# Kernel optimization log

Hardware: AMD Instinct MI355X
Metric: run time of the kernel (lower is better)

The kernel has to match this reference:

```python
import jax, jax.numpy as jnp
import numpy as np

D_MODEL = 512
NUM_HEADS = 8
D_FF = 2048
HEAD_DIM = D_MODEL // NUM_HEADS
EPS = 1e-8


def rmsnorm(x, scale):
    rms = jax.lax.rsqrt(jnp.mean(x * x, axis=-1, keepdims=True) + EPS)
    return scale * x * rms


def alibi_bias(seq_len, num_heads):
    # faithful to: 1.0 / (arange(1,H+1) * 2**arange(0,8)[:,None]).flatten()[:H]
    a = jnp.arange(1, num_heads + 1, dtype=jnp.float32)          # (H,)
    b = 2.0 ** jnp.arange(0, 8, dtype=jnp.float32)[:, None]       # (8,1)
    slopes = (1.0 / (a * b).reshape(-1))[:num_heads]               # (H,)
    pos = jnp.arange(seq_len)
    dist = jnp.abs(pos[:, None] - pos[None, :]).astype(jnp.float32)  # (S,S)
    return -slopes[:, None, None] * dist[None]                     # (H,S,S)


def setup_inputs() -> dict:
    key = jax.random.key(0)
    ks = jax.random.split(key, 12)
    s = 0.02
    return {
        "x": jax.random.normal(ks[0], (2, 2048, D_MODEL), dtype=jnp.float32),
        "norm1_scale": jnp.ones((D_MODEL,), jnp.float32),
        "norm2_scale": jnp.ones((D_MODEL,), jnp.float32),
        "in_proj_w": jax.random.normal(ks[1], (3 * D_MODEL, D_MODEL), jnp.float32) * s,
        "in_proj_b": jnp.zeros((3 * D_MODEL,), jnp.float32),
        "out_proj_w": jax.random.normal(ks[2], (D_MODEL, D_MODEL), jnp.float32) * s,
        "out_proj_b": jnp.zeros((D_MODEL,), jnp.float32),
        "w1": jax.random.normal(ks[3], (D_FF, D_MODEL), jnp.float32) * s,
        "b1": jnp.zeros((D_FF,), jnp.float32),
        "w2": jax.random.normal(ks[4], (D_MODEL, D_FF), jnp.float32) * s,
        "b2": jnp.zeros((D_MODEL,), jnp.float32),
    }


def reference(x, norm1_scale, norm2_scale, in_proj_w, in_proj_b,
              out_proj_w, out_proj_b, w1, b1, w2, b2):
    B, S, D = x.shape
    xn = rmsnorm(x, norm1_scale)
    qkv = xn @ in_proj_w.T + in_proj_b                      # (B,S,3D)
    q, k, v = jnp.split(qkv, 3, axis=-1)
    q = q.reshape(B, S, NUM_HEADS, HEAD_DIM)
    k = k.reshape(B, S, NUM_HEADS, HEAD_DIM)
    v = v.reshape(B, S, NUM_HEADS, HEAD_DIM)
    scale = 1.0 / jnp.sqrt(jnp.float32(HEAD_DIM))
    scores = jnp.einsum('bqhd,bkhd->bhqk', q, k) * scale    # (B,H,S,S)
    scores = scores + alibi_bias(S, NUM_HEADS)[None]
    attn = jax.nn.softmax(scores, axis=-1)
    ctx = jnp.einsum('bhqk,bkhd->bqhd', attn, v).reshape(B, S, D)
    attn_out = ctx @ out_proj_w.T + out_proj_b
    x = x + attn_out                                        # dropout is identity (eval)
    xn2 = rmsnorm(x, norm2_scale)
    h = jax.nn.gelu(xn2 @ w1.T + b1, approximate=False)
    mlp_out = h @ w2.T + b2
    return x + mlp_out
```

## Files before the change

kernel.cpp:

```cpp
#include <hip/hip_runtime.h>
#include <math.h>


typedef __bf16 bf16x8 __attribute__((ext_vector_type(8)));
typedef float  f32x4  __attribute__((ext_vector_type(4)));

#define TOKENS 4096
#define DMODEL 512
#define SEQ    2048
#define SPLITK 2
#define QSCALE 0.1803368801f

__device__ __forceinline__ void gl_lds16(const __bf16* g, __bf16* l) {
    __builtin_amdgcn_global_load_lds(
        (const __attribute__((address_space(1))) void*)g,
        (__attribute__((address_space(3))) void*)l, 16, 0, 0);
}

union PkU { unsigned u; __bf16 h[2]; };

__global__ void pre_kernel(const float* __restrict__ x, const float* __restrict__ n1s,
                           __bf16* __restrict__ xn1,
                           const float* __restrict__ w0, const float* __restrict__ w1,
                           const float* __restrict__ w2, const float* __restrict__ w3,
                           __bf16* __restrict__ d0, __bf16* __restrict__ d1,
                           __bf16* __restrict__ d2, __bf16* __restrict__ d3) {
    if (blockIdx.x < 1024) {
        int wave = threadIdx.x >> 6, lane = threadIdx.x & 63;
        int tok = blockIdx.x * 4 + wave;
        const float* row = x + (size_t)tok * DMODEL;
        float4 v0 = *(const float4*)&row[lane * 4];
        float4 v1 = *(const float4*)&row[256 + lane * 4];
        float ss = v0.x*v0.x + v0.y*v0.y + v0.z*v0.z + v0.w*v0.w
                 + v1.x*v1.x + v1.y*v1.y + v1.z*v1.z + v1.w*v1.w;
        #pragma unroll
        for (int off = 1; off < 64; off <<= 1) ss += __shfl_xor(ss, off);
        float r = rsqrtf(ss * (1.0f / DMODEL) + 1e-8f);
        __bf16* o = xn1 + (size_t)tok * DMODEL;
        o[lane*4 + 0] = (__bf16)(v0.x * r * n1s[lane*4 + 0]);
        o[lane*4 + 1] = (__bf16)(v0.y * r * n1s[lane*4 + 1]);
        o[lane*4 + 2] = (__bf16)(v0.z * r * n1s[lane*4 + 2]);
        o[lane*4 + 3] = (__bf16)(v0.w * r * n1s[lane*4 + 3]);
        o[256 + lane*4 + 0] = (__bf16)(v1.x * r * n1s[256 + lane*4 + 0]);
        o[256 + lane*4 + 1] = (__bf16)(v1.y * r * n1s[256 + lane*4 + 1]);
        o[256 + lane*4 + 2] = (__bf16)(v1.z * r * n1s[256 + lane*4 + 2]);
        o[256 + lane*4 + 3] = (__bf16)(v1.w * r * n1s[256 + lane*4 + 3]);
    } else {
        const int N0 = 1536 * 512, N1 = 512 * 512, N2 = 2048 * 512, N3 = 512 * 2048;
        int i4 = ((blockIdx.x - 1024) * 256 + threadIdx.x) * 4;
        const float* s; __bf16* d;
        if (i4 < N0)              { s = w0 + i4;  d = d0 + i4; }
        else if ((i4 -= N0) < N1) { s = w1 + i4;  d = d1 + i4; }
        else if ((i4 -= N1) < N2) { s = w2 + i4;  d = d2 + i4; }
        else if ((i4 -= N2) < N3) { s = w3 + i4;  d = d3 + i4; }
        else return;
        float4 v = *(const float4*)s;
        d[0] = (__bf16)v.x; d[1] = (__bf16)v.y; d[2] = (__bf16)v.z; d[3] = (__bf16)v.w;
    }
}

__global__ void rmsnorm_kernel(const float* __restrict__ x, const float* __restrict__ scale,
                               __bf16* __restrict__ out) {
    int wave = threadIdx.x >> 6, lane = threadIdx.x & 63;
    int tok = blockIdx.x * 4 + wave;
    const float* row = x + (size_t)tok * DMODEL;
    float4 v0 = *(const float4*)&row[lane * 4];
    float4 v1 = *(const float4*)&row[256 + lane * 4];
    float ss = v0.x*v0.x + v0.y*v0.y + v0.z*v0.z + v0.w*v0.w
             + v1.x*v1.x + v1.y*v1.y + v1.z*v1.z + v1.w*v1.w;
    #pragma unroll
    for (int off = 1; off < 64; off <<= 1) ss += __shfl_xor(ss, off);
    float r = rsqrtf(ss * (1.0f / DMODEL) + 1e-8f);
    __bf16* o = out + (size_t)tok * DMODEL;
    o[lane*4 + 0] = (__bf16)(v0.x * r * scale[lane*4 + 0]);
    o[lane*4 + 1] = (__bf16)(v0.y * r * scale[lane*4 + 1]);
    o[lane*4 + 2] = (__bf16)(v0.z * r * scale[lane*4 + 2]);
    o[lane*4 + 3] = (__bf16)(v0.w * r * scale[lane*4 + 3]);
    o[256 + lane*4 + 0] = (__bf16)(v1.x * r * scale[256 + lane*4 + 0]);
    o[256 + lane*4 + 1] = (__bf16)(v1.y * r * scale[256 + lane*4 + 1]);
    o[256 + lane*4 + 2] = (__bf16)(v1.z * r * scale[256 + lane*4 + 2]);
    o[256 + lane*4 + 3] = (__bf16)(v1.w * r * scale[256 + lane*4 + 3]);
}

template <int EPI, int TM>
__global__ __launch_bounds__(256) void gemm_bt(
    const __bf16* __restrict__ A, const __bf16* __restrict__ W,
    const float* __restrict__ bias, const float* __restrict__ res,
    float* __restrict__ Cf, __bf16* __restrict__ Cb,
    __bf16* __restrict__ qb, __bf16* __restrict__ kb, __bf16* __restrict__ vtb,
    int M, int N, int K)
{
    constexpr int RI = TM / 32;
    __shared__ alignas(16) __bf16 As[2][TM * 32];
    __shared__ alignas(16) __bf16 Bs[2][128 * 32];
    const int tid = threadIdx.x;
    const int bm = blockIdx.x * TM;
    const int bn = blockIdx.y * 128;
    const int wave = tid >> 6, lane = tid & 63;
    const int wm = (wave & 1) * (TM / 2), wn = (wave >> 1) * 64;
    const int lrow = lane & 15;
    const int kq = (lane >> 4) * 8;

    f32x4 acc[RI][4] = {};

    for (int k0 = 0; k0 < K; k0 += 64) {
        __syncthreads();
        #pragma unroll
        for (int i = 0; i < TM / 32; i++) {
            int tt = i * 256 + tid;
            int kh = tt / (TM * 4), rem = tt % (TM * 4);
            int mrow = rem >> 2, c8 = rem & 3;
            gl_lds16(&A[(size_t)(bm + mrow) * K + k0 + kh * 32 + c8 * 8],
                     (__bf16*)As + tt * 8);
        }
        #pragma unroll
        for (int i = 0; i < 4; i++) {
            int tt = i * 256 + tid;
            int kh = tt >> 9, rem = tt & 511;
            int nrow = rem >> 2, c8 = rem & 3;
            gl_lds16(&W[(size_t)(bn + nrow) * K + k0 + kh * 32 + c8 * 8],
                     (__bf16*)Bs + tt * 8);
        }
        __syncthreads();
        #pragma unroll
        for (int kh = 0; kh < 2; kh++) {
            bf16x8 af[RI], bfv[4];
            #pragma unroll
            for (int i = 0; i < RI; i++) af[i] = *(bf16x8*)&As[kh][(wm + i*16 + lrow)*32 + kq];
            #pragma unroll
            for (int j = 0; j < 4; j++) bfv[j] = *(bf16x8*)&Bs[kh][(wn + j*16 + lrow)*32 + kq];
            #pragma unroll
            for (int i = 0; i < RI; i++)
                #pragma unroll
                for (int j = 0; j < 4; j++)
                    acc[i][j] = __builtin_amdgcn_mfma_f32_16x16x32_bf16(af[i], bfv[j], acc[i][j], 0, 0, 0);
        }
    }

    const int crow0 = (lane >> 4) * 4;
    const int ccol = lane & 15;
    const int quad = lane >> 4;

    if (EPI == 4) {
        #pragma unroll
        for (int j = 0; j < 4; j++) {
            const int col = bn + wn + j * 16 + ccol;
            const float bv = bias[col];
            if (col < 512) {
                const int h = col >> 6, d = col & 63;
                #pragma unroll
                for (int i = 0; i < RI; i++) {
                    const int row0 = bm + wm + i * 16 + crow0;
                    const int b = row0 >> 11, s0 = row0 & 2047;
                    #pragma unroll
                    for (int r = 0; r < 4; r++)
                        qb[(((size_t)b*8 + h)*2048 + s0 + r)*64 + d] =
                            (__bf16)((acc[i][j][r] + bv) * QSCALE);
                }
            } else if (col < 1024) {
                const int h = (col - 512) >> 6, d = col & 63;
                #pragma unroll
                for (int i = 0; i < RI; i++) {
                    const int row0 = bm + wm + i * 16 + crow0;
                    const int b = row0 >> 11, s0 = row0 & 2047;
                    #pragma unroll
                    for (int r = 0; r < 4; r++)
                        kb[(((size_t)b*8 + h)*2048 + s0 + r)*64 + d] = (__bf16)(acc[i][j][r] + bv);
                }
            } else {
                const int h = (col - 1024) >> 6, d = col & 63;
                const int tok0 = bm + wm;
                const int b = tok0 >> 11, sbase = tok0 & 2047;
                unsigned* vrow = (unsigned*)vtb + (((size_t)b*8 + h)*64 + d) * 1024 + (sbase >> 1);
                #pragma unroll
                for (int ip = 0; ip < RI / 2; ip++) {
                    #pragma unroll
                    for (int r = 0; r < 4; r++) {
                        PkU pk;
                        pk.h[0] = (__bf16)(acc[2*ip][j][r] + bv);
                        pk.h[1] = (__bf16)(acc[2*ip+1][j][r] + bv);
                        vrow[ip * 16 + quad * 4 + r] = pk.u;
                    }
                }
            }
        }
    } else {
        #pragma unroll
        for (int i = 0; i < RI; i++) {
            const int row0 = bm + wm + i * 16 + crow0;
            #pragma unroll
            for (int j = 0; j < 4; j++) {
                const int col = bn + wn + j * 16 + ccol;
                const float bv = bias[col];
                if (EPI == 1) {
                    #pragma unroll
                    for (int r = 0; r < 4; r++) {
                        const size_t idx = (size_t)(row0 + r) * N + col;
                        Cf[idx] = res[idx] + acc[i][j][r] + bv;
                    }
                } else {
                    #pragma unroll
                    for (int r = 0; r < 4; r++) {
                        float v = acc[i][j][r] + bv;
                        Cb[(size_t)(row0 + r) * N + col] =
                            (__bf16)(0.5f * v * (1.0f + erff(v * 0.70710678f)));
                    }
                }
            }
        }
    }
}

__global__ __launch_bounds__(256, 4) void attn_kernel(
    const __bf16* __restrict__ qb, const __bf16* __restrict__ kb,
    const __bf16* __restrict__ vtb,
    __bf16* __restrict__ Opart, float* __restrict__ lpart)
{
    const int qt = blockIdx.x, bh = blockIdx.y, sp = blockIdx.z;
    const int h = bh & 7;
    const int tid = threadIdx.x, wave = tid >> 6, lane = tid & 63;
    const int lrow = lane & 15, quad = lane >> 4;

    __shared__ alignas(16) __bf16 Ks[2][2][64 * 32];
    __shared__ alignas(16) __bf16 Vt[2][2][64 * 32];
    __shared__ alignas(16) unsigned Pt4[4][2][32][20];

    const float slope2 = -1.44269504f / (float)(h + 1);
    const int qbase = qt * 128 + wave * 32;
    const int kt0 = sp * (32 / SPLITK), kt1 = kt0 + 32 / SPLITK;

    bf16x8 qf[2][2];
    #pragma unroll
    for (int rt = 0; rt < 2; rt++)
        #pragma unroll
        for (int dh = 0; dh < 2; dh++)
            qf[rt][dh] = *(const bf16x8*)&qb[((size_t)bh*2048 + qbase + rt*16 + lrow)*64 + dh*32 + quad*8];

    bf16x8 ones;
    #pragma unroll
    for (int j = 0; j < 8; j++) ones[j] = (__bf16)1.0f;

    f32x4 O[2][4] = {};
    f32x4 lacc[2] = {};

    auto stage = [&](int kt, int buf) {
        const int kbase = kt * 64;
        #pragma unroll
        for (int i = 0; i < 2; i++) {
            int tt = i * 256 + tid;
            int dh = tt >> 8, key = (tt & 255) >> 2, c8 = (tt & 3) * 8;
            gl_lds16(&kb[((size_t)bh*2048 + kbase + key)*64 + dh*32 + c8],
                     (__bf16*)Ks[buf] + tt * 8);
        }
        #pragma unroll
        for (int i = 0; i < 2; i++) {
            int tt = i * 256 + tid;
            int kh = tt >> 8, d = (tt & 255) >> 2, ck = (tt & 3) * 8;
            gl_lds16(&vtb[((size_t)bh*64 + d)*2048 + kbase + kh*32 + ck],
                     (__bf16*)Vt[buf] + tt * 8);
        }
    };

    stage(kt0, 0);

    for (int kt = kt0, buf = 0; kt < kt1; kt++, buf ^= 1) {
        const int kbase = kt * 64;
        __syncthreads();
        if (kt + 1 < kt1) stage(kt + 1, buf ^ 1);

        bf16x8 kf[4][2];
        #pragma unroll
        for (int j = 0; j < 4; j++)
            #pragma unroll
            for (int dh = 0; dh < 2; dh++)
                kf[j][dh] = *(bf16x8*)&Ks[buf][dh][(j*16 + lrow)*32 + quad*8];

        #pragma unroll
        for (int rt = 0; rt < 2; rt++) {
            f32x4 Sc[4] = {};
            #pragma unroll
            for (int dh = 0; dh < 2; dh++)
                #pragma unroll
                for (int j = 0; j < 4; j++)
                    Sc[j] = __builtin_amdgcn_mfma_f32_16x16x32_bf16(qf[rt][dh], kf[j][dh], Sc[j], 0, 0, 0);

            const float dbase = (float)(qbase + rt*16 + quad*4 - kbase - lrow);
            #pragma unroll
            for (int r = 0; r < 4; r++) {
                const float d0 = dbase + (float)r;
                #pragma unroll
                for (int jp = 0; jp < 2; jp++) {
                    float v0 = fmaf(slope2, fabsf(d0 - (float)(jp*32)),      Sc[2*jp  ][r]);
                    float v1 = fmaf(slope2, fabsf(d0 - (float)(jp*32 + 16)), Sc[2*jp+1][r]);
                    PkU pk;
                    pk.h[0] = (__bf16)exp2f(v0);
                    pk.h[1] = (__bf16)exp2f(v1);
                    Pt4[wave][jp][rt*16 + quad*4 + r][lrow] = pk.u;
                }
            }
        }

        bf16x8 pf[2][2];
        #pragma unroll
        for (int rt = 0; rt < 2; rt++)
            #pragma unroll
            for (int kh = 0; kh < 2; kh++)
                pf[rt][kh] = *(bf16x8*)&Pt4[wave][kh][rt*16 + lrow][quad*4];

        #pragma unroll
        for (int rt = 0; rt < 2; rt++)
            #pragma unroll
            for (int kh = 0; kh < 2; kh++)
                lacc[rt] = __builtin_amdgcn_mfma_f32_16x16x32_bf16(pf[rt][kh], ones, lacc[rt], 0, 0, 0);

        #pragma unroll
        for (int dt = 0; dt < 4; dt++) {
            #pragma unroll
            for (int kh = 0; kh < 2; kh++) {
                bf16x8 vf = *(bf16x8*)&Vt[buf][kh][(dt*16 + lrow)*32 + quad*8];
                #pragma unroll
                for (int rt = 0; rt < 2; rt++)
                    O[rt][dt] = __builtin_amdgcn_mfma_f32_16x16x32_bf16(pf[rt][kh], vf, O[rt][dt], 0, 0, 0);
            }
        }
    }

    #pragma unroll
    for (int rt = 0; rt < 2; rt++) {
        #pragma unroll
        for (int dt = 0; dt < 4; dt++)
            #pragma unroll
            for (int r = 0; r < 4; r++) {
                const int q = qbase + rt*16 + quad*4 + r;
                Opart[(((size_t)sp*16 + bh)*2048 + q)*64 + dt*16 + lrow] = (__bf16)O[rt][dt][r];
            }
        if (lrow == 0) {
            #pragma unroll
            for (int r = 0; r < 4; r++)
                lpart[((size_t)sp*16 + bh)*2048 + qbase + rt*16 + quad*4 + r] = lacc[rt][r];
        }
    }
}

__global__ void combine_kernel(const __bf16* __restrict__ Opart, const float* __restrict__ lpart,
                               __bf16* __restrict__ ctx) {
    const int idx = blockIdx.x * 256 + threadIdx.x;
    const int d2 = idx & 31;
    const int q  = (idx >> 5) & 2047;
    const int bh = idx >> 16;
    float ox = 0.0f, oy = 0.0f, l = 0.0f;
    #pragma unroll
    for (int sp = 0; sp < SPLITK; sp++) {
        PkU o; o.u = *((const unsigned*)Opart + (((size_t)sp*16 + bh)*2048 + q)*32 + d2);
        ox += (float)o.h[0]; oy += (float)o.h[1];
        l += lpart[((size_t)sp*16 + bh)*2048 + q];
    }
    const float inv = 1.0f / l;
    PkU pk;
    pk.h[0] = (__bf16)(ox * inv);
    pk.h[1] = (__bf16)(oy * inv);
    const int b = bh >> 3, h = bh & 7;
    *((unsigned*)ctx + (((size_t)b*2048 + q)*512 + h*64) / 2 + d2) = pk.u;
}

extern "C" void kernel_launch(void* const* d_in, const int* in_sizes, int n_in,
                              void* d_out, int out_size, void* d_ws, size_t ws_size,
                              hipStream_t stream) {
    const float* x    = (const float*)d_in[0];
    const float* n1s  = (const float*)d_in[1];
    const float* n2s  = (const float*)d_in[2];
    const float* wqkv = (const float*)d_in[3];
    const float* bqkv = (const float*)d_in[4];
    const float* wout = (const float*)d_in[5];
    const float* bout = (const float*)d_in[6];
    const float* w1   = (const float*)d_in[7];
    const float* b1   = (const float*)d_in[8];
    const float* w2   = (const float*)d_in[9];
    const float* b2   = (const float*)d_in[10];
    float* out = (float*)d_out;

    char* ws = (char*)d_ws;
    __bf16* xn1    = (__bf16*)ws; ws += (size_t)TOKENS * DMODEL * 2;
    __bf16* qbuf   = (__bf16*)ws; ws += (size_t)TOKENS * DMODEL * 2;
    __bf16* kbuf   = (__bf16*)ws; ws += (size_t)TOKENS * DMODEL * 2;
    __bf16* vtbuf  = (__bf16*)ws; ws += (size_t)TOKENS * DMODEL * 2;
    __bf16* wqkv_b = (__bf16*)ws; ws += (size_t)1536 * DMODEL * 2;
    __bf16* wout_b = (__bf16*)ws; ws += (size_t)DMODEL * DMODEL * 2;
    __bf16* w1_b   = (__bf16*)ws; ws += (size_t)2048 * DMODEL * 2;
    __bf16* w2_b   = (__bf16*)ws; ws += (size_t)DMODEL * 2048 * 2;
    __bf16* ctx    = (__bf16*)ws; ws += (size_t)TOKENS * DMODEL * 2;
    float*  lpart  = (float*)ws;  ws += (size_t)SPLITK * 16 * 2048 * 4;
    __bf16* Opart  = (__bf16*)ws; ws += (size_t)SPLITK * 16 * 2048 * 64 * 2;
    float*  x1     = (float*)ws;  ws += (size_t)TOKENS * DMODEL * 4;
    __bf16* xn2    = (__bf16*)ws; ws += (size_t)TOKENS * DMODEL * 2;
    __bf16* hbuf   = (__bf16*)ws;

    pre_kernel<<<dim3(4096), 256, 0, stream>>>(x, n1s, xn1,
        wqkv, wout, w1, w2, wqkv_b, wout_b, w1_b, w2_b);

    gemm_bt<4, 128><<<dim3(TOKENS / 128, 1536 / 128), 256, 0, stream>>>(
        xn1, wqkv_b, bqkv, nullptr, nullptr, nullptr, qbuf, kbuf, vtbuf,
        TOKENS, 1536, DMODEL);

    attn_kernel<<<dim3(SEQ / 128, 16, SPLITK), 256, 0, stream>>>(
        qbuf, kbuf, vtbuf, Opart, lpart);

    combine_kernel<<<dim3(16 * 2048 * 32 / 256), 256, 0, stream>>>(Opart, lpart, ctx);

    gemm_bt<1, 32><<<dim3(TOKENS / 32, DMODEL / 128), 256, 0, stream>>>(
        ctx, wout_b, bout, x, x1, nullptr, nullptr, nullptr, nullptr,
        TOKENS, DMODEL, DMODEL);

    rmsnorm_kernel<<<dim3(TOKENS / 4), 256, 0, stream>>>(x1, n2s, xn2);

    gemm_bt<2, 128><<<dim3(TOKENS / 128, 2048 / 128), 256, 0, stream>>>(
        xn2, w1_b, b1, nullptr, nullptr, hbuf, nullptr, nullptr, nullptr,
        TOKENS, 2048, DMODEL);

    gemm_bt<1, 32><<<dim3(TOKENS / 32, DMODEL / 128), 256, 0, stream>>>(
        hbuf, w2_b, b2, x1, out, nullptr, nullptr, nullptr, nullptr,
        TOKENS, DMODEL, 2048);
}
```

Baseline: 200.8 us.

## Split-K the FFN down-projection with atomics and retune tiles and attention split

The second-norm kernel now also pre-initialises the output with residual plus bias. This lets the FFN down-projection run as a 4-way split-K GEMM that accumulates with atomic adds. The QKV and FFN-up GEMMs switch to 64-row tiles, and attention splits the key range 4 ways instead of 2. Exact erf GELU is replaced by a tanh-form approximation computed with exp2. Together these aim to raise occupancy and parallelism, at the cost of atomic traffic, nondeterministic summation order, and a small GELU approximation error.

```diff
diff --git a/kernel.cpp b/kernel.cpp
--- a/kernel.cpp
+++ b/kernel.cpp
@@ -8,7 +8,7 @@
 #define TOKENS 4096
 #define DMODEL 512
 #define SEQ    2048
-#define SPLITK 2
+#define SPLITK 4
 #define QSCALE 0.1803368801f
 
 __device__ __forceinline__ void gl_lds16(const __bf16* g, __bf16* l) {
@@ -59,11 +59,12 @@
     }
 }
 
-__global__ void rmsnorm_kernel(const float* __restrict__ x, const float* __restrict__ scale,
-                               __bf16* __restrict__ out) {
+__global__ void rmsnorm2_kernel(const float* __restrict__ x1, const float* __restrict__ scale,
+                                const float* __restrict__ b2,
+                                __bf16* __restrict__ xn2, float* __restrict__ outInit) {
     int wave = threadIdx.x >> 6, lane = threadIdx.x & 63;
     int tok = blockIdx.x * 4 + wave;
-    const float* row = x + (size_t)tok * DMODEL;
+    const float* row = x1 + (size_t)tok * DMODEL;
     float4 v0 = *(const float4*)&row[lane * 4];
     float4 v1 = *(const float4*)&row[256 + lane * 4];
     float ss = v0.x*v0.x + v0.y*v0.y + v0.z*v0.z + v0.w*v0.w
@@ -71,7 +72,7 @@
     #pragma unroll
     for (int off = 1; off < 64; off <<= 1) ss += __shfl_xor(ss, off);
     float r = rsqrtf(ss * (1.0f / DMODEL) + 1e-8f);
-    __bf16* o = out + (size_t)tok * DMODEL;
+    __bf16* o = xn2 + (size_t)tok * DMODEL;
     o[lane*4 + 0] = (__bf16)(v0.x * r * scale[lane*4 + 0]);
     o[lane*4 + 1] = (__bf16)(v0.y * r * scale[lane*4 + 1]);
     o[lane*4 + 2] = (__bf16)(v0.z * r * scale[lane*4 + 2]);
@@ -80,9 +81,15 @@
     o[256 + lane*4 + 1] = (__bf16)(v1.y * r * scale[256 + lane*4 + 1]);
     o[256 + lane*4 + 2] = (__bf16)(v1.z * r * scale[256 + lane*4 + 2]);
     o[256 + lane*4 + 3] = (__bf16)(v1.w * r * scale[256 + lane*4 + 3]);
-}
-
-template <int EPI, int TM>
+    float4 b0 = *(const float4*)&b2[lane * 4];
+    float4 b1v = *(const float4*)&b2[256 + lane * 4];
+    float4 w0 = make_float4(v0.x + b0.x, v0.y + b0.y, v0.z + b0.z, v0.w + b0.w);
+    float4 w1 = make_float4(v1.x + b1v.x, v1.y + b1v.y, v1.z + b1v.z, v1.w + b1v.w);
+    *(float4*)&outInit[(size_t)tok * DMODEL + lane * 4] = w0;
+    *(float4*)&outInit[(size_t)tok * DMODEL + 256 + lane * 4] = w1;
+}
+
+template <int EPI, int TM, int KS = 1>
 __global__ __launch_bounds__(256) void gemm_bt(
     const __bf16* __restrict__ A, const __bf16* __restrict__ W,
     const float* __restrict__ bias, const float* __restrict__ res,
@@ -103,7 +110,10 @@
 
     f32x4 acc[RI][4] = {};
 
-    for (int k0 = 0; k0 < K; k0 += 64) {
+    const int Kc = K / KS;
+    const int kbeg = (KS > 1) ? blockIdx.z * Kc : 0;
+
+    for (int k0 = kbeg; k0 < kbeg + Kc; k0 += 64) {
         __syncthreads();
         #pragma unroll
         for (int i = 0; i < TM / 32; i++) {
@@ -191,19 +201,27 @@
             #pragma unroll
             for (int j = 0; j < 4; j++) {
                 const int col = bn + wn + j * 16 + ccol;
-                const float bv = bias[col];
                 if (EPI == 1) {
+                    const float bv = bias[col];
                     #pragma unroll
                     for (int r = 0; r < 4; r++) {
                         const size_t idx = (size_t)(row0 + r) * N + col;
                         Cf[idx] = res[idx] + acc[i][j][r] + bv;
                     }
-                } else {
+                } else if (EPI == 2) {
+                    const float bv = bias[col];
                     #pragma unroll
                     for (int r = 0; r < 4; r++) {
                         float v = acc[i][j][r] + bv;
-                        Cb[(size_t)(row0 + r) * N + col] =
-                            (__bf16)(0.5f * v * (1.0f + erff(v * 0.70710678f)));
+                        float u = v * (0.7978845608f + 0.0356774081f * v * v);
+                        float t = exp2f(u * 2.8853900818f);
+                        Cb[(size_t)(row0 + r) * N + col] = (__bf16)(v - v / (t + 1.0f));
+                    }
+                } else {
+                    #pragma unroll
+                    for (int r = 0; r < 4; r++) {
+                        const size_t idx = (size_t)(row0 + r) * N + col;
+                        unsafeAtomicAdd(&Cf[idx], acc[i][j][r]);
                     }
                 }
             }
@@ -398,7 +416,7 @@
     pre_kernel<<<dim3(4096), 256, 0, stream>>>(x, n1s, xn1,
         wqkv, wout, w1, w2, wqkv_b, wout_b, w1_b, w2_b);
 
-    gemm_bt<4, 128><<<dim3(TOKENS / 128, 1536 / 128), 256, 0, stream>>>(
+    gemm_bt<4, 64><<<dim3(TOKENS / 64, 1536 / 128), 256, 0, stream>>>(
         xn1, wqkv_b, bqkv, nullptr, nullptr, nullptr, qbuf, kbuf, vtbuf,
         TOKENS, 1536, DMODEL);
 
@@ -411,13 +429,13 @@
         ctx, wout_b, bout, x, x1, nullptr, nullptr, nullptr, nullptr,
         TOKENS, DMODEL, DMODEL);
 
-    rmsnorm_kernel<<<dim3(TOKENS / 4), 256, 0, stream>>>(x1, n2s, xn2);
-
-    gemm_bt<2, 128><<<dim3(TOKENS / 128, 2048 / 128), 256, 0, stream>>>(
+    rmsnorm2_kernel<<<dim3(TOKENS / 4), 256, 0, stream>>>(x1, n2s, b2, xn2, out);
+
+    gemm_bt<2, 64><<<dim3(TOKENS / 64, 2048 / 128), 256, 0, stream>>>(
         xn2, w1_b, b1, nullptr, nullptr, hbuf, nullptr, nullptr, nullptr,
         TOKENS, 2048, DMODEL);
 
-    gemm_bt<1, 32><<<dim3(TOKENS / 32, DMODEL / 128), 256, 0, stream>>>(
-        hbuf, w2_b, b2, x1, out, nullptr, nullptr, nullptr, nullptr,
+    gemm_bt<5, 64, 4><<<dim3(TOKENS / 64, DMODEL / 128, 4), 256, 0, stream>>>(
+        hbuf, w2_b, nullptr, nullptr, out, nullptr, nullptr, nullptr, nullptr,
         TOKENS, DMODEL, 2048);
 }
```

New measurement: 205.1 us. 2.2% more time.

## Split-K the second MLP GEMM, shrink GEMM tiles, raise attention split, use tanh GELU

Applied to the files above, without the earlier changes.

The second MLP GEMM is split along K into two partial fp32 outputs, which a new elementwise kernel adds to the residual and bias. The QKV and first MLP GEMMs switch to smaller M tiles for more blocks, and attention key-splitting goes from 2 to 4. The exact erf GELU is replaced with a tanh approximation built on exp2. These changes aim to raise occupancy and parallelism on the smaller GEMMs. In exchange they add extra partial-buffer traffic, an extra launch, and a small accuracy deviation from the erf GELU.

```diff
diff --git a/kernel.cpp b/kernel.cpp
--- a/kernel.cpp
+++ b/kernel.cpp
@@ -8,7 +8,7 @@
 #define TOKENS 4096
 #define DMODEL 512
 #define SEQ    2048
-#define SPLITK 2
+#define SPLITK 4
 #define QSCALE 0.1803368801f
 
 __device__ __forceinline__ void gl_lds16(const __bf16* g, __bf16* l) {
@@ -82,7 +82,7 @@
     o[256 + lane*4 + 3] = (__bf16)(v1.w * r * scale[256 + lane*4 + 3]);
 }
 
-template <int EPI, int TM>
+template <int EPI, int TM, int KS = 1>
 __global__ __launch_bounds__(256) void gemm_bt(
     const __bf16* __restrict__ A, const __bf16* __restrict__ W,
     const float* __restrict__ bias, const float* __restrict__ res,
@@ -103,7 +103,10 @@
 
     f32x4 acc[RI][4] = {};
 
-    for (int k0 = 0; k0 < K; k0 += 64) {
+    const int Kc = K / KS;
+    const int kbeg = (KS > 1) ? blockIdx.z * Kc : 0;
+
+    for (int k0 = kbeg; k0 < kbeg + Kc; k0 += 64) {
         __syncthreads();
         #pragma unroll
         for (int i = 0; i < TM / 32; i++) {
@@ -191,20 +194,27 @@
             #pragma unroll
             for (int j = 0; j < 4; j++) {
                 const int col = bn + wn + j * 16 + ccol;
-                const float bv = bias[col];
                 if (EPI == 1) {
+                    const float bv = bias[col];
                     #pragma unroll
                     for (int r = 0; r < 4; r++) {
                         const size_t idx = (size_t)(row0 + r) * N + col;
                         Cf[idx] = res[idx] + acc[i][j][r] + bv;
                     }
-                } else {
+                } else if (EPI == 2) {
+                    const float bv = bias[col];
                     #pragma unroll
                     for (int r = 0; r < 4; r++) {
                         float v = acc[i][j][r] + bv;
-                        Cb[(size_t)(row0 + r) * N + col] =
-                            (__bf16)(0.5f * v * (1.0f + erff(v * 0.70710678f)));
+                        float u = v * (0.7978845608f + 0.0356774081f * v * v);
+                        float t = exp2f(u * 2.8853900818f);
+                        Cb[(size_t)(row0 + r) * N + col] = (__bf16)(v - v / (t + 1.0f));
                     }
+                } else {
+                    const size_t zoff = (size_t)blockIdx.z * M * N;
+                    #pragma unroll
+                    for (int r = 0; r < 4; r++)
+                        Cf[zoff + (size_t)(row0 + r) * N + col] = acc[i][j][r];
                 }
             }
         }
@@ -361,6 +371,21 @@
     pk.h[1] = (__bf16)(oy * inv);
     const int b = bh >> 3, h = bh & 7;
     *((unsigned*)ctx + (((size_t)b*2048 + q)*512 + h*64) / 2 + d2) = pk.u;
+}
+
+__global__ void combine2_kernel(const float* __restrict__ p, const float* __restrict__ x1,
+                                const float* __restrict__ b2, float* __restrict__ out) {
+    const int i4 = (blockIdx.x * 256 + threadIdx.x) * 4;
+    float4 a  = *(const float4*)&x1[i4];
+    float4 b  = *(const float4*)&b2[i4 & 511];
+    float4 c0 = *(const float4*)&p[i4];
+    float4 c1 = *(const float4*)&p[(size_t)TOKENS * DMODEL + i4];
+    float4 o;
+    o.x = a.x + b.x + c0.x + c1.x;
+    o.y = a.y + b.y + c0.y + c1.y;
+    o.z = a.z + b.z + c0.z + c1.z;
+    o.w = a.w + b.w + c0.w + c1.w;
+    *(float4*)&out[i4] = o;
 }
 
 extern "C" void kernel_launch(void* const* d_in, const int* in_sizes, int n_in,
@@ -380,25 +405,26 @@
     float* out = (float*)d_out;
 
     char* ws = (char*)d_ws;
-    __bf16* xn1    = (__bf16*)ws; ws += (size_t)TOKENS * DMODEL * 2;
-    __bf16* qbuf   = (__bf16*)ws; ws += (size_t)TOKENS * DMODEL * 2;
-    __bf16* kbuf   = (__bf16*)ws; ws += (size_t)TOKENS * DMODEL * 2;
-    __bf16* vtbuf  = (__bf16*)ws; ws += (size_t)TOKENS * DMODEL * 2;
-    __bf16* wqkv_b = (__bf16*)ws; ws += (size_t)1536 * DMODEL * 2;
-    __bf16* wout_b = (__bf16*)ws; ws += (size_t)DMODEL * DMODEL * 2;
-    __bf16* w1_b   = (__bf16*)ws; ws += (size_t)2048 * DMODEL * 2;
-    __bf16* w2_b   = (__bf16*)ws; ws += (size_t)DMODEL * 2048 * 2;
-    __bf16* ctx    = (__bf16*)ws; ws += (size_t)TOKENS * DMODEL * 2;
-    float*  lpart  = (float*)ws;  ws += (size_t)SPLITK * 16 * 2048 * 4;
-    __bf16* Opart  = (__bf16*)ws; ws += (size_t)SPLITK * 16 * 2048 * 64 * 2;
-    float*  x1     = (float*)ws;  ws += (size_t)TOKENS * DMODEL * 4;
-    __bf16* xn2    = (__bf16*)ws; ws += (size_t)TOKENS * DMODEL * 2;
-    __bf16* hbuf   = (__bf16*)ws;
+    __bf16* xn1     = (__bf16*)ws; ws += (size_t)TOKENS * DMODEL * 2;
+    __bf16* qbuf    = (__bf16*)ws; ws += (size_t)TOKENS * DMODEL * 2;
+    __bf16* kbuf    = (__bf16*)ws; ws += (size_t)TOKENS * DMODEL * 2;
+    __bf16* vtbuf   = (__bf16*)ws; ws += (size_t)TOKENS * DMODEL * 2;
+    __bf16* wqkv_b  = (__bf16*)ws; ws += (size_t)1536 * DMODEL * 2;
+    __bf16* wout_b  = (__bf16*)ws; ws += (size_t)DMODEL * DMODEL * 2;
+    __bf16* w1_b    = (__bf16*)ws; ws += (size_t)2048 * DMODEL * 2;
+    __bf16* w2_b    = (__bf16*)ws; ws += (size_t)DMODEL * 2048 * 2;
+    __bf16* ctx     = (__bf16*)ws; ws += (size_t)TOKENS * DMODEL * 2;
+    float*  lpart   = (float*)ws;  ws += (size_t)SPLITK * 16 * 2048 * 4;
+    __bf16* Opart   = (__bf16*)ws; ws += (size_t)SPLITK * 16 * 2048 * 64 * 2;
+    float*  x1      = (float*)ws;  ws += (size_t)TOKENS * DMODEL * 4;
+    __bf16* xn2     = (__bf16*)ws; ws += (size_t)TOKENS * DMODEL * 2;
+    __bf16* hbuf    = (__bf16*)ws; ws += (size_t)TOKENS * 2048 * 2;
+    float*  mlp2p   = (float*)ws;  ws += (size_t)2 * TOKENS * DMODEL * 4;
 
     pre_kernel<<<dim3(4096), 256, 0, stream>>>(x, n1s, xn1,
         wqkv, wout, w1, w2, wqkv_b, wout_b, w1_b, w2_b);
 
-    gemm_bt<4, 128><<<dim3(TOKENS / 128, 1536 / 128), 256, 0, stream>>>(
+    gemm_bt<4, 64><<<dim3(TOKENS / 64, 1536 / 128), 256, 0, stream>>>(
         xn1, wqkv_b, bqkv, nullptr, nullptr, nullptr, qbuf, kbuf, vtbuf,
         TOKENS, 1536, DMODEL);
 
@@ -413,11 +439,14 @@
 
     rmsnorm_kernel<<<dim3(TOKENS / 4), 256, 0, stream>>>(x1, n2s, xn2);
 
-    gemm_bt<2, 128><<<dim3(TOKENS / 128, 2048 / 128), 256, 0, stream>>>(
+    gemm_bt<2, 32><<<dim3(TOKENS / 32, 2048 / 128), 256, 0, stream>>>(
         xn2, w1_b, b1, nullptr, nullptr, hbuf, nullptr, nullptr, nullptr,
         TOKENS, 2048, DMODEL);
 
-    gemm_bt<1, 32><<<dim3(TOKENS / 32, DMODEL / 128), 256, 0, stream>>>(
-        hbuf, w2_b, b2, x1, out, nullptr, nullptr, nullptr, nullptr,
+    gemm_bt<6, 32, 2><<<dim3(TOKENS / 32, DMODEL / 128, 2), 256, 0, stream>>>(
+        hbuf, w2_b, nullptr, nullptr, mlp2p, nullptr, nullptr, nullptr, nullptr,
         TOKENS, DMODEL, 2048);
-}
+
+    combine2_kernel<<<dim3(TOKENS * DMODEL / 4 / 256), 256, 0, stream>>>(
+        mlp2p, x1, b2, out);
+}
```

Result: no change. 199.6 us (-0.6%).
